# Performance work log

Hardware: AMD Instinct MI355X
Metric: run time of the kernel (lower is better)

## Reference

```python
import jax, jax.numpy as jnp
import numpy as np

N_NODES = 50000
N_EDGES = 800000
NODE_DIM = 64
HIDDEN = 128
OUT_DIM = 256
N_LAYERS = 3


def setup_inputs() -> dict:
    key = jax.random.key(0)
    ks = jax.random.split(key, 12)
    inp = {
        'x': jax.random.normal(ks[0], (N_NODES, NODE_DIM), dtype=jnp.float32),
        'src': jax.random.randint(ks[1], (N_EDGES,), 0, N_NODES, dtype=jnp.int32),
        'dst': jax.random.randint(ks[2], (N_EDGES,), 0, N_NODES, dtype=jnp.int32),
        'Wp': jax.random.normal(ks[3], (NODE_DIM, HIDDEN), dtype=jnp.float32) / np.sqrt(NODE_DIM),
        'bp': jax.random.normal(ks[4], (HIDDEN,), dtype=jnp.float32) * 0.01,
        'Wg': jax.random.normal(ks[5], (N_LAYERS, HIDDEN, HIDDEN), dtype=jnp.float32) / np.sqrt(HIDDEN),
        'bg': jax.random.normal(ks[6], (N_LAYERS, HIDDEN), dtype=jnp.float32) * 0.01,
        'W1': jax.random.normal(ks[7], (HIDDEN, HIDDEN), dtype=jnp.float32) / np.sqrt(HIDDEN),
        'b1': jax.random.normal(ks[8], (HIDDEN,), dtype=jnp.float32) * 0.01,
        'W2': jax.random.normal(ks[9], (HIDDEN, OUT_DIM), dtype=jnp.float32) / np.sqrt(HIDDEN),
        'b2': jax.random.normal(ks[10], (OUT_DIM,), dtype=jnp.float32) * 0.01,
    }
    return inp


def reference(x, src, dst, Wp, bp, Wg, bg, W1, b1, W2, b2):
    n = x.shape[0]
    # node_proj
    h = x @ Wp + bp  # [N, H]
    # in-degree per dst node; zero-degree nodes keep a zero message
    deg = jax.ops.segment_sum(jnp.ones_like(src, dtype=h.dtype), dst, num_segments=n)  # [N]
    inv_deg = jnp.where(deg > 0, 1.0 / jnp.maximum(deg, 1.0), 0.0)[:, None]  # [N,1]
    for l in range(Wg.shape[0]):
        # gather neighbor embeddings along edges, mean-aggregate into dst
        msg = jax.ops.segment_sum(h[src], dst, num_segments=n) * inv_deg  # [N, H]
        h = jax.nn.relu(h + msg @ Wg[l] + bg[l])
    g = jnp.mean(h, axis=0)  # [H]
    latent = jax.nn.relu(g @ W1 + b1) @ W2 + b2  # [OUT_DIM]
    return latent
```

## Files before the change

kernel.cpp:

```cpp
#include <hip/hip_runtime.h>
#include <hip/hip_fp16.h>

#define H   128
#define ND  64
#define TILE_R 64
#define CAP 64
#define NSCAT 2048

typedef _Float16 f16x8 __attribute__((ext_vector_type(8)));
typedef float    f32x4 __attribute__((ext_vector_type(4)));

__device__ __forceinline__ unsigned short f2h(float f) {
  return __half_as_ushort(__float2half(f));
}
__device__ __forceinline__ float h2f(unsigned short u) {
  return __half2float(__ushort_as_half(u));
}


__global__ __launch_bounds__(256) void prep_all_k(const float* __restrict__ Wg,
                                                  const float* __restrict__ Wp,
                                                  unsigned short* __restrict__ wfrag,
                                                  unsigned short* __restrict__ wpfrag,
                                                  int* __restrict__ cnt, int n_pad,
                                                  float* __restrict__ gsum,
                                                  int* __restrict__ done) {
  __shared__ float sW[H * H];
  if (blockIdx.x < 3) {
    const float* W = Wg + (size_t)blockIdx.x * H * H;
    for (int i = threadIdx.x; i < H * H; i += 256) sW[i] = W[i];
    __syncthreads();
    unsigned short* out = wfrag + (size_t)blockIdx.x * 2048 * 8;
    for (int c = threadIdx.x; c < 2048; c += 256) {
      int lane = c & 63, combo = c >> 6;
      int it = combo >> 2, ks = combo & 3;
      int nc = it * 16 + (lane & 15);
      int kb = ks * 32 + (lane >> 4) * 8;
      unsigned short* o = out + (size_t)c * 8;
#pragma unroll
      for (int j = 0; j < 8; ++j) o[j] = f2h(sW[(kb + j) * H + nc]);
    }
  } else if (blockIdx.x == 3) {
    for (int i = threadIdx.x; i < ND * H; i += 256) sW[i] = Wp[i];
    __syncthreads();
    for (int c = threadIdx.x; c < 1024; c += 256) {
      int lane = c & 63, combo = c >> 6;
      int it = combo >> 1, ks = combo & 1;
      int nc = it * 16 + (lane & 15);
      int kb = ks * 32 + (lane >> 4) * 8;
      unsigned short* o = wpfrag + (size_t)c * 8;
#pragma unroll
      for (int j = 0; j < 8; ++j) o[j] = f2h(sW[(kb + j) * H + nc]);
    }
  } else {
    int zb = blockIdx.x - 4;
    int chunk = (n_pad + 15) >> 4;
    int lo = zb * chunk, hi = lo + chunk; if (hi > n_pad) hi = n_pad;
    for (int i = lo + threadIdx.x; i < hi; i += 256) cnt[i] = 0;
    if (zb == 0) {
      if (threadIdx.x < H) gsum[threadIdx.x] = 0.f;
      if (threadIdx.x == 0) *done = 0;
    }
  }
}


__global__ __launch_bounds__(256) void scatter_proj_k(
    const int* __restrict__ src, const int* __restrict__ dst,
    int* __restrict__ cnt, unsigned short* __restrict__ ssrc, int E, int psz,
    const float* __restrict__ x, const unsigned short* __restrict__ wpfrag,
    const float* __restrict__ bp, unsigned short* __restrict__ hout, int n) {
  __shared__ unsigned short sB[1024 * 8];
  if ((int)blockIdx.x < NSCAT) {
    int grp = blockIdx.x & 7;
    int lo = grp * psz, hi = lo + psz;
    int stride = (NSCAT >> 3) * 256;
    for (int e = ((int)blockIdx.x >> 3) * 256 + (int)threadIdx.x; e < E; e += stride) {
      int d = dst[e];
      if (d >= lo && d < hi) {
        int p = atomicAdd(&cnt[d], 1);
        if (p < CAP) ssrc[(size_t)d * CAP + p] = (unsigned short)src[e];
      }
    }
    return;
  }

  uint4* sB4 = (uint4*)sB;
  const uint4* wsrc = (const uint4*)wpfrag;
  for (int i = threadIdx.x; i < 1024; i += 256) sB4[i] = wsrc[i];
  __syncthreads();

  int wave = threadIdx.x >> 6, lane = threadIdx.x & 63;
  int quad = lane >> 4, n16 = lane & 15;
  int node = ((int)blockIdx.x - NSCAT) * 64 + wave * 16 + n16;

  union { unsigned short s[8]; uint4 u; f16x8 h; } bm[2];
  if (node < n) {
    const float* xr = x + (size_t)node * ND;
#pragma unroll
    for (int ks = 0; ks < 2; ++ks) {
      const float* pk = xr + ks * 32 + quad * 8;
      float4 A0 = *(const float4*)pk;
      float4 A1 = *(const float4*)(pk + 4);
      bm[ks].s[0] = f2h(A0.x); bm[ks].s[1] = f2h(A0.y);
      bm[ks].s[2] = f2h(A0.z); bm[ks].s[3] = f2h(A0.w);
      bm[ks].s[4] = f2h(A1.x); bm[ks].s[5] = f2h(A1.y);
      bm[ks].s[6] = f2h(A1.z); bm[ks].s[7] = f2h(A1.w);
    }
  } else {
    bm[0].u = make_uint4(0, 0, 0, 0);
    bm[1].u = make_uint4(0, 0, 0, 0);
  }

  f32x4 acc[8] = {};
#pragma unroll
  for (int it = 0; it < 8; ++it) {
#pragma unroll
    for (int ks = 0; ks < 2; ++ks) {
      union { uint4 u; f16x8 h; } aw;
      aw.u = sB4[(it * 2 + ks) * 64 + lane];
      acc[it] = __builtin_amdgcn_mfma_f32_16x16x32_f16(aw.h, bm[ks].h, acc[it], 0, 0, 0);
    }
  }

  unsigned short* rout = hout + (size_t)node * H;
#pragma unroll
  for (int it = 0; it < 8; ++it) {
    int f0 = it * 16 + quad * 4;
    float4 bv = *(const float4*)(bp + f0);
    ushort4 o = make_ushort4(f2h(acc[it][0] + bv.x), f2h(acc[it][1] + bv.y),
                             f2h(acc[it][2] + bv.z), f2h(acc[it][3] + bv.w));
    *(ushort4*)(rout + f0) = o;
  }
}


__global__ __launch_bounds__(256) void aggregate_w_k(
    const unsigned short* __restrict__ hin,
    const int* __restrict__ cnt,
    const unsigned short* __restrict__ ssrc,
    unsigned short* __restrict__ msgh, int n) {
  int node = blockIdx.x * 4 + (threadIdx.x >> 6);
  if (node >= n) return;
  int l = threadIdx.x & 63;
  int sub = l >> 4, li = l & 15;
  int deg = cnt[node]; if (deg > CAP) deg = CAP;
  const __half2 z = __floats2half2_rn(0.f, 0.f);
  __half2 acc[4] = {z, z, z, z};
  if (deg > 0) {
    int eid = (int)ssrc[(size_t)node * CAP + (l < deg ? l : 0)];
    int j = 0;
#pragma unroll 4
    for (; j + 4 <= deg; j += 4) {
      int s = __shfl(eid, j + sub, 64);
      union { uint4 u; __half2 h[4]; } v;
      v.u = *(const uint4*)(hin + (size_t)s * H + li * 8);
      acc[0] = __hadd2(acc[0], v.h[0]);
      acc[1] = __hadd2(acc[1], v.h[1]);
      acc[2] = __hadd2(acc[2], v.h[2]);
      acc[3] = __hadd2(acc[3], v.h[3]);
    }
    if (j < deg) {
      int jj = j + sub;
      int s = __shfl(eid, jj < deg ? jj : deg - 1, 64);
      if (jj < deg) {
        union { uint4 u; __half2 h[4]; } v;
        v.u = *(const uint4*)(hin + (size_t)s * H + li * 8);
        acc[0] = __hadd2(acc[0], v.h[0]);
        acc[1] = __hadd2(acc[1], v.h[1]);
        acc[2] = __hadd2(acc[2], v.h[2]);
        acc[3] = __hadd2(acc[3], v.h[3]);
      }
    }
  }
#pragma unroll
  for (int k = 0; k < 4; ++k) {
    union { __half2 h; unsigned int u; } a, b, c;
    a.h = acc[k];
    b.u = __shfl_xor(a.u, 16, 64);
    a.h = __hadd2(a.h, b.h);
    c.u = __shfl_xor(a.u, 32, 64);
    acc[k] = __hadd2(a.h, c.h);
  }
  if (sub == 0) {
    float inv = (deg > 0) ? 1.0f / (float)deg : 0.f;
    uint4 o;
    unsigned int* op = (unsigned int*)&o;
#pragma unroll
    for (int k = 0; k < 4; ++k) {
      float lo = __low2float(acc[k]) * inv;
      float hi = __high2float(acc[k]) * inv;
      op[k] = (unsigned int)f2h(lo) | ((unsigned int)f2h(hi) << 16);
    }
    *(uint4*)(msgh + (size_t)node * H + li * 8) = o;
  }
}


__global__ __launch_bounds__(256, 4) void update_mfma_k(
    const unsigned short* __restrict__ hin,
    unsigned short* __restrict__ hout,
    const unsigned short* __restrict__ msgh,
    const unsigned short* __restrict__ wfrag,
    const float* __restrict__ bg, int n) {
  __shared__ unsigned short sB[2048 * 8];
  uint4* sB4 = (uint4*)sB;
  const uint4* wsrc = (const uint4*)wfrag;
  for (int i = threadIdx.x; i < 2048; i += 256) sB4[i] = wsrc[i];
  __syncthreads();

  int wave = threadIdx.x >> 6, lane = threadIdx.x & 63;
  int quad = lane >> 4, n16 = lane & 15;
  int node = blockIdx.x * 64 + wave * 16 + n16;

  union { uint4 u; f16x8 h; } bm[4];
  const unsigned short* mrow = msgh + (size_t)node * H;
#pragma unroll
  for (int ks = 0; ks < 4; ++ks)
    bm[ks].u = *(const uint4*)(mrow + ks * 32 + quad * 8);

  f32x4 acc[8] = {};
#pragma unroll
  for (int it = 0; it < 8; ++it) {
#pragma unroll
    for (int ks = 0; ks < 4; ++ks) {
      union { uint4 u; f16x8 h; } aw;
      aw.u = sB4[(it * 4 + ks) * 64 + lane];
      acc[it] = __builtin_amdgcn_mfma_f32_16x16x32_f16(aw.h, bm[ks].h, acc[it], 0, 0, 0);
    }
  }

  const unsigned short* rin = hin + (size_t)node * H;
  unsigned short* rout = hout + (size_t)node * H;
#pragma unroll
  for (int it = 0; it < 8; ++it) {
    int f0 = it * 16 + quad * 4;
    float4 bv = *(const float4*)(bg + f0);
    ushort4 old = *(const ushort4*)(rin + f0);
    float v0 = h2f(old.x) + acc[it][0] + bv.x; v0 = v0 > 0.f ? v0 : 0.f;
    float v1 = h2f(old.y) + acc[it][1] + bv.y; v1 = v1 > 0.f ? v1 : 0.f;
    float v2 = h2f(old.z) + acc[it][2] + bv.z; v2 = v2 > 0.f ? v2 : 0.f;
    float v3 = h2f(old.w) + acc[it][3] + bv.w; v3 = v3 > 0.f ? v3 : 0.f;
    *(ushort4*)(rout + f0) = make_ushort4(f2h(v0), f2h(v1), f2h(v2), f2h(v3));
  }
}


__global__ __launch_bounds__(256) void pool_mlp_k(
    const unsigned short* __restrict__ hb, float* __restrict__ gsum,
    int* __restrict__ done,
    const float* __restrict__ W1, const float* __restrict__ b1,
    const float* __restrict__ W2, const float* __restrict__ b2,
    float* __restrict__ out, float invN, int n, int nblocks) {
  int c  = threadIdx.x & 31;
  int rg = threadIdx.x >> 5;
  float4 acc = {0.f, 0.f, 0.f, 0.f};
#pragma unroll 4
  for (int row = blockIdx.x * 8 + rg; row < n; row += gridDim.x * 8) {
    ushort4 v = ((const ushort4*)(hb + (size_t)row * H))[c];
    acc.x += h2f(v.x); acc.y += h2f(v.y);
    acc.z += h2f(v.z); acc.w += h2f(v.w);
  }
  __shared__ float4 s[256];
  s[threadIdx.x] = acc;
  __syncthreads();
  if (threadIdx.x < 32) {
    float4 t = s[c];
#pragma unroll
    for (int k = 1; k < 8; ++k) {
      float4 q = s[k * 32 + c];
      t.x += q.x; t.y += q.y; t.z += q.z; t.w += q.w;
    }
    atomicAdd(&gsum[c * 4 + 0], t.x);
    atomicAdd(&gsum[c * 4 + 1], t.y);
    atomicAdd(&gsum[c * 4 + 2], t.z);
    atomicAdd(&gsum[c * 4 + 3], t.w);
  }
  __threadfence();
  __syncthreads();
  __shared__ int lastflag;
  if (threadIdx.x == 0)
    lastflag = (atomicAdd(done, 1) == nblocks - 1) ? 1 : 0;
  __syncthreads();
  if (!lastflag) return;

  __shared__ float g[H];
  __shared__ float hid[H];
  __shared__ float hpart[256];
  int tid = threadIdx.x;
  if (tid < H) g[tid] = atomicAdd(&gsum[tid], 0.0f) * invN;
  __syncthreads();
  {
    int o = tid & 127, half = tid >> 7;
    int k0 = half * 64;
    float p0 = 0.f, p1 = 0.f, p2 = 0.f, p3 = 0.f;
#pragma unroll
    for (int k = 0; k < 64; k += 4) {
      p0 += g[k0 + k + 0] * W1[(k0 + k + 0) * H + o];
      p1 += g[k0 + k + 1] * W1[(k0 + k + 1) * H + o];
      p2 += g[k0 + k + 2] * W1[(k0 + k + 2) * H + o];
      p3 += g[k0 + k + 3] * W1[(k0 + k + 3) * H + o];
    }
    hpart[tid] = (p0 + p1) + (p2 + p3);
  }
  __syncthreads();
  if (tid < H) {
    float v = hpart[tid] + hpart[tid + 128] + b1[tid];
    hid[tid] = v > 0.f ? v : 0.f;
  }
  __syncthreads();
  {
    float q0 = 0.f, q1 = 0.f, q2 = 0.f, q3 = 0.f;
#pragma unroll
    for (int k = 0; k < H; k += 4) {
      q0 += hid[k + 0] * W2[(k + 0) * 256 + tid];
      q1 += hid[k + 1] * W2[(k + 1) * 256 + tid];
      q2 += hid[k + 2] * W2[(k + 2) * 256 + tid];
      q3 += hid[k + 3] * W2[(k + 3) * 256 + tid];
    }
    out[tid] = b2[tid] + (q0 + q1) + (q2 + q3);
  }
}


extern "C" void kernel_launch(void* const* d_in, const int* in_sizes, int n_in,
                              void* d_out, int out_size, void* d_ws, size_t ws_size,
                              hipStream_t stream) {
  const float* x  = (const float*)d_in[0];
  const int*   src = (const int*)d_in[1];
  const int*   dst = (const int*)d_in[2];
  const float* Wp = (const float*)d_in[3];
  const float* bp = (const float*)d_in[4];
  const float* Wg = (const float*)d_in[5];
  const float* bg = (const float*)d_in[6];
  const float* W1 = (const float*)d_in[7];
  const float* b1 = (const float*)d_in[8];
  const float* W2 = (const float*)d_in[9];
  const float* b2 = (const float*)d_in[10];
  float* out = (float*)d_out;

  const int N = in_sizes[0] / ND;
  const int E = in_sizes[1];
  const int N_pad = ((N + TILE_R - 1) / TILE_R) * TILE_R;
  const size_t NH = (size_t)N_pad * H;
  const int psz = (N_pad + 7) / 8;

  char* p = (char*)d_ws;
  unsigned short* hb0   = (unsigned short*)p; p += NH * sizeof(unsigned short);
  unsigned short* hb1   = (unsigned short*)p; p += NH * sizeof(unsigned short);
  unsigned short* msgh  = (unsigned short*)p; p += NH * sizeof(unsigned short);
  unsigned short* wfrag = (unsigned short*)p; p += 3 * 2048 * 8 * sizeof(unsigned short);
  unsigned short* wpfrag= (unsigned short*)p; p += 1024 * 8 * sizeof(unsigned short);
  unsigned short* ssrc  = (unsigned short*)p; p += (size_t)N_pad * CAP * sizeof(unsigned short);
  int*   cnt  = (int*)p;   p += (size_t)N_pad * sizeof(int);
  float* gsum = (float*)p; p += H * sizeof(float);
  int*   done = (int*)p;   p += sizeof(int);

  const int ntiles = N_pad / TILE_R;
  const int POOLB = 256;

  prep_all_k<<<20, 256, 0, stream>>>(Wg, Wp, wfrag, wpfrag, cnt, N_pad, gsum, done);

  scatter_proj_k<<<NSCAT + ntiles, 256, 0, stream>>>(src, dst, cnt, ssrc, E, psz,
                                                     x, wpfrag, bp, hb0, N);

  unsigned short* hin = hb0;
  unsigned short* hout = hb1;
  for (int l = 0; l < 3; ++l) {
    aggregate_w_k<<<(N + 3) / 4, 256, 0, stream>>>(hin, cnt, ssrc, msgh, N);
    update_mfma_k<<<ntiles, 256, 0, stream>>>(hin, hout, msgh,
                                              wfrag + (size_t)l * 2048 * 8,
                                              bg + (size_t)l * H, N);
    unsigned short* t = hin; hin = hout; hout = t;
  }

  pool_mlp_k<<<POOLB, 256, 0, stream>>>(hin, gsum, done, W1, b1, W2, b2, out,
                                        1.0f / (float)N, N, POOLB);
}
```

Before: 294.2 us.

## Fuse neighbor aggregation into the MFMA update kernel via swizzled LDS messages

Merges the per-layer aggregate and update kernels into one: each block gathers and mean-reduces neighbor rows for its 64 nodes, processing two nodes per wave iteration, and writes the messages into an XOR-swizzled shared-memory tile that feeds the MFMA matmul directly. This removes the global message buffer round trip and one launch per layer. In exchange only 782 blocks do the gather, which cuts the parallelism available to hide gather latency. Separately, the edge scatter now loads dst as 4-wide vectors with 4 chunks per thread; edges in a final partial group of 4 are dropped, which is harmless only when E is a multiple of 4.

After: 403.9 us. 1.37x slower.

```diff
diff --git a/kernel.cpp b/kernel.cpp
--- a/kernel.cpp
+++ b/kernel.cpp
@@ -9,12 +9,17 @@
 
 typedef _Float16 f16x8 __attribute__((ext_vector_type(8)));
 typedef float    f32x4 __attribute__((ext_vector_type(4)));
+typedef int      i32x4 __attribute__((ext_vector_type(4)));
 
 __device__ __forceinline__ unsigned short f2h(float f) {
   return __half_as_ushort(__float2half(f));
 }
 __device__ __forceinline__ float h2f(unsigned short u) {
   return __half2float(__ushort_as_half(u));
+}
+
+__device__ __forceinline__ int smoff(int row, int col16) {
+  return row * H + (((col16) ^ (row & 15)) << 3);
 }
 
 
@@ -74,12 +79,25 @@
   if ((int)blockIdx.x < NSCAT) {
     int grp = blockIdx.x & 7;
     int lo = grp * psz, hi = lo + psz;
-    int stride = (NSCAT >> 3) * 256;
-    for (int e = ((int)blockIdx.x >> 3) * 256 + (int)threadIdx.x; e < E; e += stride) {
-      int d = dst[e];
-      if (d >= lo && d < hi) {
-        int p = atomicAdd(&cnt[d], 1);
-        if (p < CAP) ssrc[(size_t)d * CAP + p] = (unsigned short)src[e];
+    int base = ((int)blockIdx.x >> 3) * 1024 + (int)threadIdx.x * 4;
+    const int S = (NSCAT >> 3) * 1024;
+    i32x4 dd[4];
+    int   ee[4];
+#pragma unroll
+    for (int t = 0; t < 4; ++t) {
+      ee[t] = base + t * S;
+      if (ee[t] + 4 <= E) dd[t] = *(const i32x4*)(dst + ee[t]);
+      else                dd[t] = (i32x4){-1, -1, -1, -1};
+    }
+#pragma unroll
+    for (int t = 0; t < 4; ++t) {
+#pragma unroll
+      for (int j = 0; j < 4; ++j) {
+        int d = dd[t][j];
+        if (d >= lo && d < hi) {
+          int p = atomicAdd(&cnt[d], 1);
+          if (p < CAP) ssrc[(size_t)d * CAP + p] = (unsigned short)src[ee[t] + j];
+        }
       }
     }
     return;
@@ -135,89 +153,88 @@
 }
 
 
-__global__ __launch_bounds__(256) void aggregate_w_k(
+__global__ __launch_bounds__(256) void layer_fused_k(
     const unsigned short* __restrict__ hin,
+    unsigned short* __restrict__ hout,
     const int* __restrict__ cnt,
     const unsigned short* __restrict__ ssrc,
-    unsigned short* __restrict__ msgh, int n) {
-  int node = blockIdx.x * 4 + (threadIdx.x >> 6);
-  if (node >= n) return;
-  int l = threadIdx.x & 63;
-  int sub = l >> 4, li = l & 15;
-  int deg = cnt[node]; if (deg > CAP) deg = CAP;
-  const __half2 z = __floats2half2_rn(0.f, 0.f);
-  __half2 acc[4] = {z, z, z, z};
-  if (deg > 0) {
-    int eid = (int)ssrc[(size_t)node * CAP + (l < deg ? l : 0)];
-    int j = 0;
-#pragma unroll 4
-    for (; j + 4 <= deg; j += 4) {
-      int s = __shfl(eid, j + sub, 64);
-      union { uint4 u; __half2 h[4]; } v;
-      v.u = *(const uint4*)(hin + (size_t)s * H + li * 8);
-      acc[0] = __hadd2(acc[0], v.h[0]);
-      acc[1] = __hadd2(acc[1], v.h[1]);
-      acc[2] = __hadd2(acc[2], v.h[2]);
-      acc[3] = __hadd2(acc[3], v.h[3]);
-    }
-    if (j < deg) {
-      int jj = j + sub;
-      int s = __shfl(eid, jj < deg ? jj : deg - 1, 64);
-      if (jj < deg) {
-        union { uint4 u; __half2 h[4]; } v;
-        v.u = *(const uint4*)(hin + (size_t)s * H + li * 8);
-        acc[0] = __hadd2(acc[0], v.h[0]);
-        acc[1] = __hadd2(acc[1], v.h[1]);
-        acc[2] = __hadd2(acc[2], v.h[2]);
-        acc[3] = __hadd2(acc[3], v.h[3]);
-      }
-    }
-  }
-#pragma unroll
-  for (int k = 0; k < 4; ++k) {
-    union { __half2 h; unsigned int u; } a, b, c;
-    a.h = acc[k];
-    b.u = __shfl_xor(a.u, 16, 64);
-    a.h = __hadd2(a.h, b.h);
-    c.u = __shfl_xor(a.u, 32, 64);
-    acc[k] = __hadd2(a.h, c.h);
-  }
-  if (sub == 0) {
-    float inv = (deg > 0) ? 1.0f / (float)deg : 0.f;
-    uint4 o;
-    unsigned int* op = (unsigned int*)&o;
-#pragma unroll
-    for (int k = 0; k < 4; ++k) {
-      float lo = __low2float(acc[k]) * inv;
-      float hi = __high2float(acc[k]) * inv;
-      op[k] = (unsigned int)f2h(lo) | ((unsigned int)f2h(hi) << 16);
-    }
-    *(uint4*)(msgh + (size_t)node * H + li * 8) = o;
-  }
-}
-
-
-__global__ __launch_bounds__(256, 4) void update_mfma_k(
-    const unsigned short* __restrict__ hin,
-    unsigned short* __restrict__ hout,
-    const unsigned short* __restrict__ msgh,
     const unsigned short* __restrict__ wfrag,
     const float* __restrict__ bg, int n) {
-  __shared__ unsigned short sB[2048 * 8];
-  uint4* sB4 = (uint4*)sB;
+  __shared__ unsigned short sW[2048 * 8];
+  __shared__ unsigned short sM[64 * H];
+  uint4* sW4 = (uint4*)sW;
   const uint4* wsrc = (const uint4*)wfrag;
-  for (int i = threadIdx.x; i < 2048; i += 256) sB4[i] = wsrc[i];
-  __syncthreads();
+  for (int i = threadIdx.x; i < 2048; i += 256) sW4[i] = wsrc[i];
 
   int wave = threadIdx.x >> 6, lane = threadIdx.x & 63;
-  int quad = lane >> 4, n16 = lane & 15;
-  int node = blockIdx.x * 64 + wave * 16 + n16;
+  int sub = lane >> 4, li = lane & 15;
+  int nbase = (int)blockIdx.x * 64 + wave * 16;
+
+  const __half2 z = __floats2half2_rn(0.f, 0.f);
+#pragma unroll 1
+  for (int i = 0; i < 16; i += 2) {
+    int nodeA = nbase + i, nodeB = nbase + i + 1;
+    int degA = cnt[nodeA]; if (degA > CAP) degA = CAP;
+    int degB = cnt[nodeB]; if (degB > CAP) degB = CAP;
+    __half2 aA[4] = {z, z, z, z}, aB[4] = {z, z, z, z};
+    int eidA = (int)ssrc[(size_t)nodeA * CAP + (lane < degA ? lane : 0)];
+    int eidB = (int)ssrc[(size_t)nodeB * CAP + (lane < degB ? lane : 0)];
+    int mx = degA > degB ? degA : degB;
+    for (int j = 0; j < mx; j += 4) {
+      int jj = j + sub;
+      int sA = __shfl(eidA, jj < degA ? jj : 0, 64);
+      int sBn = __shfl(eidB, jj < degB ? jj : 0, 64);
+      if (jj < degA) {
+        union { uint4 u; __half2 h[4]; } v;
+        v.u = *(const uint4*)(hin + (size_t)sA * H + li * 8);
+        aA[0] = __hadd2(aA[0], v.h[0]); aA[1] = __hadd2(aA[1], v.h[1]);
+        aA[2] = __hadd2(aA[2], v.h[2]); aA[3] = __hadd2(aA[3], v.h[3]);
+      }
+      if (jj < degB) {
+        union { uint4 u; __half2 h[4]; } v;
+        v.u = *(const uint4*)(hin + (size_t)sBn * H + li * 8);
+        aB[0] = __hadd2(aB[0], v.h[0]); aB[1] = __hadd2(aB[1], v.h[1]);
+        aB[2] = __hadd2(aB[2], v.h[2]); aB[3] = __hadd2(aB[3], v.h[3]);
+      }
+    }
+#pragma unroll
+    for (int nn = 0; nn < 2; ++nn) {
+      __half2* ac = nn ? aB : aA;
+      int deg = nn ? degB : degA;
+      int row = (wave * 16 + i + nn);
+#pragma unroll
+      for (int k = 0; k < 4; ++k) {
+        union { __half2 h; unsigned int u; } a, b, c;
+        a.h = ac[k];
+        b.u = __shfl_xor(a.u, 16, 64);
+        a.h = __hadd2(a.h, b.h);
+        c.u = __shfl_xor(a.u, 32, 64);
+        ac[k] = __hadd2(a.h, c.h);
+      }
+      if (sub == 0) {
+        float inv = (deg > 0) ? 1.0f / (float)deg : 0.f;
+        uint4 o;
+        unsigned int* op = (unsigned int*)&o;
+#pragma unroll
+        for (int k = 0; k < 4; ++k) {
+          float lo = __low2float(ac[k]) * inv;
+          float hi = __high2float(ac[k]) * inv;
+          op[k] = (unsigned int)f2h(lo) | ((unsigned int)f2h(hi) << 16);
+        }
+        *(uint4*)&sM[smoff(row, li)] = o;
+      }
+    }
+  }
+  __syncthreads();
+
+  int quad = sub, n16 = li;
+  int row = wave * 16 + n16;
+  int node = (int)blockIdx.x * 64 + row;
 
   union { uint4 u; f16x8 h; } bm[4];
-  const unsigned short* mrow = msgh + (size_t)node * H;
 #pragma unroll
   for (int ks = 0; ks < 4; ++ks)
-    bm[ks].u = *(const uint4*)(mrow + ks * 32 + quad * 8);
+    bm[ks].u = *(const uint4*)&sM[smoff(row, ks * 4 + quad)];
 
   f32x4 acc[8] = {};
 #pragma unroll
@@ -225,7 +242,7 @@
 #pragma unroll
     for (int ks = 0; ks < 4; ++ks) {
       union { uint4 u; f16x8 h; } aw;
-      aw.u = sB4[(it * 4 + ks) * 64 + lane];
+      aw.u = sW4[(it * 4 + ks) * 64 + lane];
       acc[it] = __builtin_amdgcn_mfma_f32_16x16x32_f16(aw.h, bm[ks].h, acc[it], 0, 0, 0);
     }
   }
@@ -355,6 +372,7 @@
   int*   cnt  = (int*)p;   p += (size_t)N_pad * sizeof(int);
   float* gsum = (float*)p; p += H * sizeof(float);
   int*   done = (int*)p;   p += sizeof(int);
+  (void)msgh;
 
   const int ntiles = N_pad / TILE_R;
   const int POOLB = 256;
@@ -367,8 +385,7 @@
   unsigned short* hin = hb0;
   unsigned short* hout = hb1;
   for (int l = 0; l < 3; ++l) {
-    aggregate_w_k<<<(N + 3) / 4, 256, 0, stream>>>(hin, cnt, ssrc, msgh, N);
-    update_mfma_k<<<ntiles, 256, 0, stream>>>(hin, hout, msgh,
+    layer_fused_k<<<ntiles, 256, 0, stream>>>(hin, hout, cnt, ssrc,
                                               wfrag + (size_t)l * 2048 * 8,
                                               bg + (size_t)l * H, N);
     unsigned short* t = hin; hin = hout; hout = t;
```

## Fuse neighbor aggregation and MFMA update into one per-layer kernel

Applied to the files above, without the earlier changes.

Replaces the separate aggregate and update kernels with one 512-thread kernel per layer. Each block gathers mean messages for 16 nodes into swizzled shared memory, then runs the 128x128 MFMA update and the bias, residual and ReLU epilogue in place. This removes the global msgh write and reread and one launch per layer. In exchange, every small block reloads the full 32KB weight fragment into LDS, and the per-block node count is small.

After: 284.5 us. 3.3% less time.

```diff
diff --git a/kernel.cpp b/kernel.cpp
--- a/kernel.cpp
+++ b/kernel.cpp
@@ -15,6 +15,10 @@
 }
 __device__ __forceinline__ float h2f(unsigned short u) {
   return __half2float(__ushort_as_half(u));
+}
+
+__device__ __forceinline__ int smoff(int row, int col16) {
+  return row * H + (((col16) ^ (row & 15)) << 3);
 }
 
 
@@ -196,7 +200,6 @@
   }
 }
 
-
 __global__ __launch_bounds__(256, 4) void update_mfma_k(
     const unsigned short* __restrict__ hin,
     unsigned short* __restrict__ hout,
@@ -243,6 +246,104 @@
     float v3 = h2f(old.w) + acc[it][3] + bv.w; v3 = v3 > 0.f ? v3 : 0.f;
     *(ushort4*)(rout + f0) = make_ushort4(f2h(v0), f2h(v1), f2h(v2), f2h(v3));
   }
+}
+
+
+__global__ __launch_bounds__(512) void layer_fused512_k(
+    const unsigned short* __restrict__ hin,
+    unsigned short* __restrict__ hout,
+    const int* __restrict__ cnt,
+    const unsigned short* __restrict__ ssrc,
+    const unsigned short* __restrict__ wfrag,
+    const float* __restrict__ bg) {
+  __shared__ unsigned short sW[2048 * 8];
+  __shared__ unsigned short sM[16 * H];
+  uint4* sW4 = (uint4*)sW;
+  const uint4* wsrc = (const uint4*)wfrag;
+  for (int i = threadIdx.x; i < 2048; i += 512) sW4[i] = wsrc[i];
+
+  int wave = threadIdx.x >> 6, lane = threadIdx.x & 63;
+  int sub = lane >> 4, li = lane & 15;
+  int nbase = (int)blockIdx.x * 16;
+  int nodeA = nbase + wave * 2, nodeB = nodeA + 1;
+  int degA = cnt[nodeA]; if (degA > CAP) degA = CAP;
+  int degB = cnt[nodeB]; if (degB > CAP) degB = CAP;
+  const __half2 z = __floats2half2_rn(0.f, 0.f);
+  __half2 aA[4] = {z, z, z, z}, aB[4] = {z, z, z, z};
+  int eidA = (int)ssrc[(size_t)nodeA * CAP + (lane < degA ? lane : 0)];
+  int eidB = (int)ssrc[(size_t)nodeB * CAP + (lane < degB ? lane : 0)];
+  int mx = degA > degB ? degA : degB;
+#pragma unroll 2
+  for (int j = 0; j < mx; j += 4) {
+    int jj = j + sub;
+    int sA = __shfl(eidA, jj < degA ? jj : 0, 64);
+    int sBn = __shfl(eidB, jj < degB ? jj : 0, 64);
+    if (jj < degA) {
+      union { uint4 u; __half2 h[4]; } v;
+      v.u = *(const uint4*)(hin + (size_t)sA * H + li * 8);
+      aA[0] = __hadd2(aA[0], v.h[0]); aA[1] = __hadd2(aA[1], v.h[1]);
+      aA[2] = __hadd2(aA[2], v.h[2]); aA[3] = __hadd2(aA[3], v.h[3]);
+    }
+    if (jj < degB) {
+      union { uint4 u; __half2 h[4]; } v;
+      v.u = *(const uint4*)(hin + (size_t)sBn * H + li * 8);
+      aB[0] = __hadd2(aB[0], v.h[0]); aB[1] = __hadd2(aB[1], v.h[1]);
+      aB[2] = __hadd2(aB[2], v.h[2]); aB[3] = __hadd2(aB[3], v.h[3]);
+    }
+  }
+#pragma unroll
+  for (int nn = 0; nn < 2; ++nn) {
+    __half2* ac = nn ? aB : aA;
+    int deg = nn ? degB : degA;
+    int row = wave * 2 + nn;
+#pragma unroll
+    for (int k = 0; k < 4; ++k) {
+      union { __half2 h; unsigned int u; } a, b, c;
+      a.h = ac[k];
+      b.u = __shfl_xor(a.u, 16, 64);
+      a.h = __hadd2(a.h, b.h);
+      c.u = __shfl_xor(a.u, 32, 64);
+      ac[k] = __hadd2(a.h, c.h);
+    }
+    if (sub == 0) {
+      float inv = (deg > 0) ? 1.0f / (float)deg : 0.f;
+      uint4 o;
+      unsigned int* op = (unsigned int*)&o;
+#pragma unroll
+      for (int k = 0; k < 4; ++k) {
+        float lo = __low2float(ac[k]) * inv;
+        float hi = __high2float(ac[k]) * inv;
+        op[k] = (unsigned int)f2h(lo) | ((unsigned int)f2h(hi) << 16);
+      }
+      *(uint4*)&sM[smoff(row, li)] = o;
+    }
+  }
+  __syncthreads();
+
+  int quad = sub, n16 = li;
+  union { uint4 u; f16x8 h; } bm[4];
+#pragma unroll
+  for (int ks = 0; ks < 4; ++ks)
+    bm[ks].u = *(const uint4*)&sM[smoff(n16, ks * 4 + quad)];
+
+  f32x4 acc = {};
+#pragma unroll
+  for (int ks = 0; ks < 4; ++ks) {
+    union { uint4 u; f16x8 h; } aw;
+    aw.u = sW4[(wave * 4 + ks) * 64 + lane];
+    acc = __builtin_amdgcn_mfma_f32_16x16x32_f16(aw.h, bm[ks].h, acc, 0, 0, 0);
+  }
+
+  int node = nbase + n16;
+  int f0 = wave * 16 + quad * 4;
+  float4 bv = *(const float4*)(bg + f0);
+  ushort4 old = *(const ushort4*)(hin + (size_t)node * H + f0);
+  float v0 = h2f(old.x) + acc[0] + bv.x; v0 = v0 > 0.f ? v0 : 0.f;
+  float v1 = h2f(old.y) + acc[1] + bv.y; v1 = v1 > 0.f ? v1 : 0.f;
+  float v2 = h2f(old.z) + acc[2] + bv.z; v2 = v2 > 0.f ? v2 : 0.f;
+  float v3 = h2f(old.w) + acc[3] + bv.w; v3 = v3 > 0.f ? v3 : 0.f;
+  *(ushort4*)(hout + (size_t)node * H + f0) = make_ushort4(f2h(v0), f2h(v1),
+                                                           f2h(v2), f2h(v3));
 }
 
 
@@ -355,6 +456,7 @@
   int*   cnt  = (int*)p;   p += (size_t)N_pad * sizeof(int);
   float* gsum = (float*)p; p += H * sizeof(float);
   int*   done = (int*)p;   p += sizeof(int);
+  (void)msgh;
 
   const int ntiles = N_pad / TILE_R;
   const int POOLB = 256;
@@ -367,10 +469,9 @@
   unsigned short* hin = hb0;
   unsigned short* hout = hb1;
   for (int l = 0; l < 3; ++l) {
-    aggregate_w_k<<<(N + 3) / 4, 256, 0, stream>>>(hin, cnt, ssrc, msgh, N);
-    update_mfma_k<<<ntiles, 256, 0, stream>>>(hin, hout, msgh,
-                                              wfrag + (size_t)l * 2048 * 8,
-                                              bg + (size_t)l * H, N);
+    layer_fused512_k<<<N_pad / 16, 512, 0, stream>>>(hin, hout, cnt, ssrc,
+                                                     wfrag + (size_t)l * 2048 * 8,
+                                                     bg + (size_t)l * H);
     unsigned short* t = hin; hin = hout; hout = t;
   }
 
```
